# Optimization experiments

Measured on AMD Instinct MI355X. Metric: run time of the kernel, lower is better.

## Reference

```python
import jax, jax.numpy as jnp
import numpy as np

N_NODES = 100000

def _sage_conv(x, edge_index, w_l, b_l, w_r):
    """PyG SAGEConv with mean aggregation:
    out = lin_l(mean_{j in N(i)} x_j) + lin_r(x_i), bias only on lin_l."""
    src, dst = edge_index[0], edge_index[1]
    msgs = x[src]  # [E, d] gather
    agg = jax.ops.segment_sum(msgs, dst, num_segments=N_NODES)  # [N, d]
    cnt = jax.ops.segment_sum(jnp.ones((edge_index.shape[1],), x.dtype), dst,
                              num_segments=N_NODES)
    agg = agg / jnp.maximum(cnt, 1.0)[:, None]  # mean over neighbors
    return agg @ w_l.T + b_l + x @ w_r.T


def setup_inputs() -> dict:
    key = jax.random.key(0)
    ks = jax.random.split(key, 8)
    in_dim, hid_dim, out_dim = 128, 128, 128
    N, E = N_NODES, 1600000
    x = jax.random.normal(ks[0], (N, in_dim), dtype=jnp.float32)
    edge_index = jax.random.randint(ks[1], (2, E), 0, N, dtype=jnp.int64)
    s = 1.0 / np.sqrt(in_dim)
    w1_l = jax.random.uniform(ks[2], (hid_dim, in_dim), jnp.float32, -s, s)
    w1_r = jax.random.uniform(ks[3], (hid_dim, in_dim), jnp.float32, -s, s)
    b1 = jnp.zeros((hid_dim,), jnp.float32)
    s2 = 1.0 / np.sqrt(hid_dim)
    w2_l = jax.random.uniform(ks[4], (out_dim, hid_dim), jnp.float32, -s2, s2)
    w2_r = jax.random.uniform(ks[5], (out_dim, hid_dim), jnp.float32, -s2, s2)
    b2 = jnp.zeros((out_dim,), jnp.float32)
    return {"x": x, "edge_index": edge_index,
            "w1_l": w1_l, "b1": b1, "w1_r": w1_r,
            "w2_l": w2_l, "b2": b2, "w2_r": w2_r}


def reference(x, edge_index, w1_l, b1, w1_r, w2_l, b2, w2_r):
    h = jax.nn.relu(_sage_conv(x, edge_index, w1_l, b1, w1_r))
    # dropout rate 0.0 -> identity (eval-mode reference)
    out = _sage_conv(h, edge_index, w2_l, b2, w2_r)
    return out
```

## Files before the change

### kernel.cpp

```cpp
#include <hip/hip_runtime.h>

#define NDIM 128
#define BKT_SHIFT 9
#define BKT_NODES 512
#define BKT_CAP   12288
#define PART_CHUNK 4096

typedef unsigned short u16;
typedef unsigned char u8;
typedef unsigned int u32;
typedef __attribute__((ext_vector_type(8))) short bf16x8;
typedef __attribute__((ext_vector_type(4))) float f32x4;
typedef __attribute__((ext_vector_type(2))) float f32x2;

__device__ inline u16 f2bf(float f) {
    u32 u = __float_as_uint(f);
    u += 0x7fffu + ((u >> 16) & 1u);
    return (u16)(u >> 16);
}
__device__ inline float bf2f(u16 h) { return __uint_as_float((u32)h << 16); }

__device__ inline u8 f2q(float f) {
    u32 u = __float_as_uint(f);
    u32 s = (u >> 24) & 0x80u;
    float a = __uint_as_float(u & 0x7fffffffu);
    if (a < 0.015625f)
        return (u8)(s | (u32)__float2int_rn(a * 512.f));
    if (a >= 448.f) return (u8)(s | 0x7Eu);
    u32 ur = (u & 0x7fffffffu) + 0x7FFFFu + ((u >> 20) & 1u);
    int e = (int)(ur >> 23) - 127;
    u32 man = (ur >> 20) & 7u;
    u32 r = ((u32)(e + 7) << 3) | man;
    if (r > 0x7Eu) r = 0x7Eu;
    return (u8)(s | r);
}

#if __has_builtin(__builtin_amdgcn_cvt_pk_f32_fp8)
template<bool HI>
__device__ inline f32x2 dq2(u32 w) {
    return __builtin_amdgcn_cvt_pk_f32_fp8((int)w, HI);
}
#else
__device__ inline float dq1(u32 b) {
    int e = (b >> 3) & 15, m = b & 7, s = (b >> 7) & 1;
    int norm = e ? 1 : 0;
    float f = (float)(m + (norm << 3));
    float sc = __uint_as_float((u32)(((e ? e : 1) - 10) + 127) << 23);
    float v = f * sc;
    return s ? -v : v;
}
template<bool HI>
__device__ inline f32x2 dq2(u32 w) {
    u32 sh = HI ? 16 : 0;
    f32x2 r; r.x = dq1((w >> sh) & 0xff); r.y = dq1((w >> (sh + 8)) & 0xff);
    return r;
}
#endif


__global__ __launch_bounds__(256) void partition_kernel(
    const int* __restrict__ ei, int E,
    int* __restrict__ gcur, u32* __restrict__ ebuf) {
    __shared__ int hcnt[256];
    __shared__ int hbase[256];
    const int tid = threadIdx.x;
    const int base = blockIdx.x * PART_CHUNK;
    hcnt[tid] = 0;
    __syncthreads();

    u32 val[16];
    int bkt[16];
    #pragma unroll
    for (int k = 0; k < 16; ++k) {
        int e = base + k * 256 + tid;
        bkt[k] = -1;
        if (e < E) {
            int src = ei[e];
            int dst = ei[(size_t)E + e];
            int b = dst >> BKT_SHIFT;
            bkt[k] = b;
            val[k] = ((u32)src << BKT_SHIFT) | (u32)(dst & (BKT_NODES - 1));
            atomicAdd(&hcnt[b], 1);
        }
    }
    __syncthreads();
    {
        int c = hcnt[tid];
        if (c > 0) hbase[tid] = atomicAdd(&gcur[tid], c);
        hcnt[tid] = 0;
    }
    __syncthreads();
    #pragma unroll
    for (int k = 0; k < 16; ++k) {
        if (bkt[k] >= 0) {
            int b = bkt[k];
            int r = atomicAdd(&hcnt[b], 1);
            int off = hbase[b] + r;
            if (off < BKT_CAP)
                ebuf[(size_t)b * BKT_CAP + off] = val[k];
        }
    }
}

__global__ __launch_bounds__(256) void bucket_csr_kernel(
    const int* __restrict__ gcur, const u32* __restrict__ ebuf,
    int* __restrict__ row_beg, int* __restrict__ degN,
    int* __restrict__ col, int n) {
    __shared__ int deg_l[BKT_NODES];
    __shared__ int pre_l[BKT_NODES];
    __shared__ int cur_l[BKT_NODES];
    __shared__ int wsum[4];
    const int tid = threadIdx.x;
    const int lane = tid & 63, wid = tid >> 6;
    const int b = blockIdx.x;
    const int node0 = b << BKT_SHIFT;
    int cnt = gcur[b];
    if (cnt > BKT_CAP) cnt = BKT_CAP;
    const size_t ebase = (size_t)b * BKT_CAP;

    deg_l[tid] = 0; deg_l[tid + 256] = 0;
    cur_l[tid] = 0; cur_l[tid + 256] = 0;
    __syncthreads();

    for (int i = tid; i < cnt; i += 256)
        atomicAdd(&deg_l[ebuf[ebase + i] & (BKT_NODES - 1)], 1);
    __syncthreads();

    int v0 = deg_l[2 * tid], v1 = deg_l[2 * tid + 1];
    int s = v0 + v1, inc = s;
    #pragma unroll
    for (int d = 1; d < 64; d <<= 1) {
        int t = __shfl_up(inc, d, 64);
        if (lane >= d) inc += t;
    }
    if (lane == 63) wsum[wid] = inc;
    __syncthreads();
    int woff = 0;
    for (int w = 0; w < wid; ++w) woff += wsum[w];
    int ex = woff + (inc - s);
    pre_l[2 * tid] = ex;
    pre_l[2 * tid + 1] = ex + v0;
    __syncthreads();

    #pragma unroll
    for (int p = 0; p < 2; ++p) {
        int idx = tid + p * 256;
        int node = node0 + idx;
        if (node < n) {
            row_beg[node] = (int)ebase + pre_l[idx];
            degN[node]    = deg_l[idx];
        }
    }

    for (int i = tid; i < cnt; i += 256) {
        u32 v = ebuf[ebase + i];
        int d = v & (BKT_NODES - 1);
        int r = atomicAdd(&cur_l[d], 1);
        col[ebase + pre_l[d] + r] = (int)(v >> BKT_SHIFT);
    }
}


__global__ void build_wt_kernel(const float* __restrict__ wl,
                                const float* __restrict__ wr,
                                u16* __restrict__ wth, u16* __restrict__ wtl) {
    int idx = blockIdx.x * blockDim.x + threadIdx.x;
    if (idx >= 128 * 256) return;
    int o = idx >> 8, k = idx & 255;
    float v = (k < 128) ? wl[o * 128 + k] : wr[o * 128 + (k - 128)];
    u16 hi = f2bf(v);
    wth[idx] = hi;
    wtl[idx] = f2bf(v - bf2f(hi));
}


__global__ __launch_bounds__(256) void to_conv_kernel(
    const float* __restrict__ in, u16* __restrict__ outh,
    u8* __restrict__ outq, int n4) {
    int stride = gridDim.x * blockDim.x;
    for (int i = blockIdx.x * blockDim.x + threadIdx.x; i < n4; i += stride) {
        float4 v = *(const float4*)&in[(size_t)i * 4];
        ushort4 o;
        o.x = f2bf(v.x); o.y = f2bf(v.y); o.z = f2bf(v.z); o.w = f2bf(v.w);
        *(ushort4*)&outh[(size_t)i * 4] = o;
        u32 q = (u32)f2q(v.x) | ((u32)f2q(v.y) << 8) |
                ((u32)f2q(v.z) << 16) | ((u32)f2q(v.w) << 24);
        *(u32*)&outq[(size_t)i * 4] = q;
    }
}


__device__ inline void accumq(float acc[8], uint2 u) {
    f32x2 a;
    a = dq2<false>(u.x); acc[0] += a.x; acc[1] += a.y;
    a = dq2<true >(u.x); acc[2] += a.x; acc[3] += a.y;
    a = dq2<false>(u.y); acc[4] += a.x; acc[5] += a.y;
    a = dq2<true >(u.y); acc[6] += a.x; acc[7] += a.y;
}

__global__ __launch_bounds__(256) void aggregate_fp8_kernel(
    const u8* __restrict__ feat, const int* __restrict__ row_beg,
    const int* __restrict__ degN, const int* __restrict__ col,
    u16* __restrict__ aggh, int n) {
    int node = blockIdx.x * 16 + (threadIdx.x >> 4);
    if (node >= n) return;
    int l = threadIdx.x & 15;
    int beg = row_beg[node];
    int dg  = degN[node];
    int end = beg + dg;
    float acc[8] = {0.f, 0.f, 0.f, 0.f, 0.f, 0.f, 0.f, 0.f};
    int j = beg;
    for (; j + 8 <= end; j += 8) {
        int s[8];
        #pragma unroll
        for (int q = 0; q < 8; ++q) s[q] = col[j + q];
        uint2 u[8];
        #pragma unroll
        for (int q = 0; q < 8; ++q)
            u[q] = *(const uint2*)&feat[(size_t)s[q] * NDIM + l * 8];
        #pragma unroll
        for (int q = 0; q < 8; ++q) accumq(acc, u[q]);
    }
    if (j + 4 <= end) {
        int s[4];
        #pragma unroll
        for (int q = 0; q < 4; ++q) s[q] = col[j + q];
        uint2 u[4];
        #pragma unroll
        for (int q = 0; q < 4; ++q)
            u[q] = *(const uint2*)&feat[(size_t)s[q] * NDIM + l * 8];
        #pragma unroll
        for (int q = 0; q < 4; ++q) accumq(acc, u[q]);
        j += 4;
    }
    for (; j < end; ++j) {
        uint2 u = *(const uint2*)&feat[(size_t)col[j] * NDIM + l * 8];
        accumq(acc, u);
    }
    float inv = (dg > 0) ? 1.0f / (float)dg : 0.f;
    u16 hs[8];
    #pragma unroll
    for (int q = 0; q < 8; ++q) hs[q] = f2bf(acc[q] * inv);
    *(ushort4*)&aggh[(size_t)node * NDIM + l * 8]     = make_ushort4(hs[0], hs[1], hs[2], hs[3]);
    *(ushort4*)&aggh[(size_t)node * NDIM + l * 8 + 4] = make_ushort4(hs[4], hs[5], hs[6], hs[7]);
}


__global__ __launch_bounds__(256, 1) void gemm_bstat_kernel(
    const u16* __restrict__ aggh, const u16* __restrict__ selfh,
    const u16* __restrict__ wth, const u16* __restrict__ wtl,
    const float* __restrict__ bias,
    float* __restrict__ outF, u16* __restrict__ outH, u8* __restrict__ outQ,
    int M, int do_relu) {
    const int lane = threadIdx.x & 63;
    const int wid  = threadIdx.x >> 6;
    const int rr = lane & 15, kb = lane >> 4;
    const int ob0 = wid * 32;
    const int ntiles = (M + 15) / 16;
    const int stride = gridDim.x;

    bf16x8 WH0[8], WL0[8], WH1[8], WL1[8];
    {
        const u16* h0 = &wth[(size_t)(ob0 + rr) * 256];
        const u16* l0 = &wtl[(size_t)(ob0 + rr) * 256];
        const u16* h1 = &wth[(size_t)(ob0 + 16 + rr) * 256];
        const u16* l1 = &wtl[(size_t)(ob0 + 16 + rr) * 256];
        #pragma unroll
        for (int ks = 0; ks < 8; ++ks) {
            WH0[ks] = *(const bf16x8*)&h0[ks * 32 + kb * 8];
            WL0[ks] = *(const bf16x8*)&l0[ks * 32 + kb * 8];
            WH1[ks] = *(const bf16x8*)&h1[ks * 32 + kb * 8];
            WL1[ks] = *(const bf16x8*)&l1[ks * 32 + kb * 8];
        }
        #pragma unroll
        for (int ks = 0; ks < 8; ++ks)
            asm volatile("" : "+v"(WH0[ks]), "+v"(WL0[ks]),
                              "+v"(WH1[ks]), "+v"(WL1[ks]));
    }
    const float4 bb0 = *(const float4*)&bias[ob0 + kb * 4];
    const float4 bb1 = *(const float4*)&bias[ob0 + 16 + kb * 4];

    auto loadX = [&](bf16x8* X, int t) {
        int row = t * 16 + rr;
        if (row >= M) row = M - 1;
        const u16* ag = &aggh[(size_t)row * NDIM];
        const u16* sf = &selfh[(size_t)row * NDIM];
        #pragma unroll
        for (int ks = 0; ks < 4; ++ks) X[ks]     = *(const bf16x8*)&ag[ks * 32 + kb * 8];
        #pragma unroll
        for (int ks = 0; ks < 4; ++ks) X[4 + ks] = *(const bf16x8*)&sf[ks * 32 + kb * 8];
    };
    auto pinX = [&](bf16x8* X) {
        #pragma unroll
        for (int i = 0; i < 8; ++i) asm volatile("" : "+v"(X[i]));
    };
    auto computeStore = [&](bf16x8* X, int t) {
        f32x4 acc0 = (f32x4){0.f, 0.f, 0.f, 0.f};
        f32x4 acc1 = (f32x4){0.f, 0.f, 0.f, 0.f};
        #pragma unroll
        for (int ks = 0; ks < 8; ++ks) {
            acc0 = __builtin_amdgcn_mfma_f32_16x16x32_bf16(WH0[ks], X[ks], acc0, 0, 0, 0);
            acc0 = __builtin_amdgcn_mfma_f32_16x16x32_bf16(WL0[ks], X[ks], acc0, 0, 0, 0);
            acc1 = __builtin_amdgcn_mfma_f32_16x16x32_bf16(WH1[ks], X[ks], acc1, 0, 0, 0);
            acc1 = __builtin_amdgcn_mfma_f32_16x16x32_bf16(WL1[ks], X[ks], acc1, 0, 0, 0);
        }
        int node = t * 16 + rr;
        if (node < M) {
            float v0[4], v1[4];
            #pragma unroll
            for (int r = 0; r < 4; ++r) {
                v0[r] = acc0[r] + ((const float*)&bb0)[r];
                v1[r] = acc1[r] + ((const float*)&bb1)[r];
                if (do_relu) { v0[r] = fmaxf(v0[r], 0.f); v1[r] = fmaxf(v1[r], 0.f); }
            }
            const size_t base = (size_t)node * NDIM;
            const int oA = ob0 + kb * 4;
            const int oB = ob0 + 16 + kb * 4;
            if (outF) {
                *(float4*)&outF[base + oA] = make_float4(v0[0], v0[1], v0[2], v0[3]);
                *(float4*)&outF[base + oB] = make_float4(v1[0], v1[1], v1[2], v1[3]);
            }
            if (outH) {
                *(ushort4*)&outH[base + oA] =
                    make_ushort4(f2bf(v0[0]), f2bf(v0[1]), f2bf(v0[2]), f2bf(v0[3]));
                *(ushort4*)&outH[base + oB] =
                    make_ushort4(f2bf(v1[0]), f2bf(v1[1]), f2bf(v1[2]), f2bf(v1[3]));
            }
            if (outQ) {
                *(u32*)&outQ[base + oA] = (u32)f2q(v0[0]) | ((u32)f2q(v0[1]) << 8) |
                                          ((u32)f2q(v0[2]) << 16) | ((u32)f2q(v0[3]) << 24);
                *(u32*)&outQ[base + oB] = (u32)f2q(v1[0]) | ((u32)f2q(v1[1]) << 8) |
                                          ((u32)f2q(v1[2]) << 16) | ((u32)f2q(v1[3]) << 24);
            }
        }
    };

    bf16x8 X0[8], X1[8];
    int t = blockIdx.x;
    if (t >= ntiles) return;
    loadX(X0, t);
    while (true) {
        int tn = t + stride;
        pinX(X0);
        if (tn < ntiles) loadX(X1, tn);
        computeStore(X0, t);
        t = tn;
        if (t >= ntiles) break;
        tn = t + stride;
        pinX(X1);
        if (tn < ntiles) loadX(X0, tn);
        computeStore(X1, t);
        t = tn;
        if (t >= ntiles) break;
    }
}


extern "C" void kernel_launch(void* const* d_in, const int* in_sizes, int n_in,
                              void* d_out, int out_size, void* d_ws, size_t ws_size,
                              hipStream_t stream) {
    const float* x    = (const float*)d_in[0];
    const int*   ei   = (const int*)d_in[1];
    const float* w1_l = (const float*)d_in[2];
    const float* b1   = (const float*)d_in[3];
    const float* w1_r = (const float*)d_in[4];
    const float* w2_l = (const float*)d_in[5];
    const float* b2   = (const float*)d_in[6];
    const float* w2_r = (const float*)d_in[7];
    const int N = in_sizes[0] / NDIM;
    const int E = in_sizes[1] / 2;
    float* out = (float*)d_out;

    const int NB = (N + BKT_NODES - 1) >> BKT_SHIFT;

    char* ws = (char*)d_ws;
    size_t off = 0;
    auto take = [&](size_t bytes) -> char* {
        char* p = ws + off;
        off += (bytes + 255) & ~(size_t)255;
        return p;
    };
    int* row_beg = (int*)take((size_t)N * 4);
    int* degN    = (int*)take((size_t)N * 4);
    int* gcur    = (int*)take((size_t)NB * 4);
    u32* ebuf    = (u32*)take((size_t)NB * BKT_CAP * 4);
    int* colA    = (int*)take((size_t)NB * BKT_CAP * 4);
    u16* wt1h    = (u16*)take(128 * 256 * 2);
    u16* wt1l    = (u16*)take(128 * 256 * 2);
    u16* wt2h    = (u16*)take(128 * 256 * 2);
    u16* wt2l    = (u16*)take(128 * 256 * 2);
    u16* aggh    = (u16*)take((size_t)N * NDIM * 2);
    u16* hh      = (u16*)take((size_t)N * NDIM * 2);
    u16* xh = (u16*)d_out;
    u8*  xq = (u8*)d_out + (size_t)N * NDIM * 2;
    u8*  hq = (u8*)d_out + (size_t)N * NDIM * 3;

    (void)hipMemsetAsync(gcur, 0, (size_t)NB * 4, stream);
    partition_kernel<<<(E + PART_CHUNK - 1) / PART_CHUNK, 256, 0, stream>>>(ei, E, gcur, ebuf);
    bucket_csr_kernel<<<NB, 256, 0, stream>>>(gcur, ebuf, row_beg, degN, colA, N);
    build_wt_kernel<<<128, 256, 0, stream>>>(w1_l, w1_r, wt1h, wt1l);
    build_wt_kernel<<<128, 256, 0, stream>>>(w2_l, w2_r, wt2h, wt2l);
    to_conv_kernel<<<2048, 256, 0, stream>>>(x, xh, xq, N * NDIM / 4);

    const int gblk = 512;
    aggregate_fp8_kernel<<<(N + 15) / 16, 256, 0, stream>>>(xq, row_beg, degN, colA, aggh, N);
    gemm_bstat_kernel<<<gblk, 256, 0, stream>>>(aggh, xh, wt1h, wt1l, b1,
                                                (float*)0, hh, hq, N, 1);
    aggregate_fp8_kernel<<<(N + 15) / 16, 256, 0, stream>>>(hq, row_beg, degN, colA, aggh, N);
    gemm_bstat_kernel<<<gblk, 256, 0, stream>>>(aggh, hh, wt2h, wt2l, b2,
                                                out, (u16*)0, (u8*)0, N, 0);
}
```

Measured before the change: 212.8 us.

## Fuse neighbor aggregation into the GEMM kernel via shared-memory tile

Merges the fp8 mean-aggregation kernel and the dual-weight MFMA GEMM into one persistent kernel. Each block aggregates 16 nodes into a shared-memory bf16 tile, then feeds it straight to the MFMAs, so the intermediate aggregate buffer is never written to or read back from global memory. The cost is that the grid drops to 512 persistent blocks for the latency-bound gather, with a barrier between gather and compute and no cross-tile prefetch. The hq buffer is also moved from the output region into the workspace.

```diff
diff --git a/kernel.cpp b/kernel.cpp
--- a/kernel.cpp
+++ b/kernel.cpp
@@ -198,66 +198,22 @@
     a = dq2<true >(u.y); acc[6] += a.x; acc[7] += a.y;
 }
 
-__global__ __launch_bounds__(256) void aggregate_fp8_kernel(
-    const u8* __restrict__ feat, const int* __restrict__ row_beg,
-    const int* __restrict__ degN, const int* __restrict__ col,
-    u16* __restrict__ aggh, int n) {
-    int node = blockIdx.x * 16 + (threadIdx.x >> 4);
-    if (node >= n) return;
-    int l = threadIdx.x & 15;
-    int beg = row_beg[node];
-    int dg  = degN[node];
-    int end = beg + dg;
-    float acc[8] = {0.f, 0.f, 0.f, 0.f, 0.f, 0.f, 0.f, 0.f};
-    int j = beg;
-    for (; j + 8 <= end; j += 8) {
-        int s[8];
-        #pragma unroll
-        for (int q = 0; q < 8; ++q) s[q] = col[j + q];
-        uint2 u[8];
-        #pragma unroll
-        for (int q = 0; q < 8; ++q)
-            u[q] = *(const uint2*)&feat[(size_t)s[q] * NDIM + l * 8];
-        #pragma unroll
-        for (int q = 0; q < 8; ++q) accumq(acc, u[q]);
-    }
-    if (j + 4 <= end) {
-        int s[4];
-        #pragma unroll
-        for (int q = 0; q < 4; ++q) s[q] = col[j + q];
-        uint2 u[4];
-        #pragma unroll
-        for (int q = 0; q < 4; ++q)
-            u[q] = *(const uint2*)&feat[(size_t)s[q] * NDIM + l * 8];
-        #pragma unroll
-        for (int q = 0; q < 4; ++q) accumq(acc, u[q]);
-        j += 4;
-    }
-    for (; j < end; ++j) {
-        uint2 u = *(const uint2*)&feat[(size_t)col[j] * NDIM + l * 8];
-        accumq(acc, u);
-    }
-    float inv = (dg > 0) ? 1.0f / (float)dg : 0.f;
-    u16 hs[8];
-    #pragma unroll
-    for (int q = 0; q < 8; ++q) hs[q] = f2bf(acc[q] * inv);
-    *(ushort4*)&aggh[(size_t)node * NDIM + l * 8]     = make_ushort4(hs[0], hs[1], hs[2], hs[3]);
-    *(ushort4*)&aggh[(size_t)node * NDIM + l * 8 + 4] = make_ushort4(hs[4], hs[5], hs[6], hs[7]);
-}
-
-
-__global__ __launch_bounds__(256, 1) void gemm_bstat_kernel(
-    const u16* __restrict__ aggh, const u16* __restrict__ selfh,
+__global__ __launch_bounds__(256, 2) void fused_agg_gemm_kernel(
+    const u8* __restrict__ gatherq,
+    const u16* __restrict__ selfh,
+    const int* __restrict__ row_beg, const int* __restrict__ degN,
+    const int* __restrict__ col,
     const u16* __restrict__ wth, const u16* __restrict__ wtl,
     const float* __restrict__ bias,
     float* __restrict__ outF, u16* __restrict__ outH, u8* __restrict__ outQ,
-    int M, int do_relu) {
-    const int lane = threadIdx.x & 63;
-    const int wid  = threadIdx.x >> 6;
+    int n, int do_relu) {
+    __shared__ u16 Ah[16][136];
+    const int tid  = threadIdx.x;
+    const int lane = tid & 63;
+    const int wid  = tid >> 6;
     const int rr = lane & 15, kb = lane >> 4;
     const int ob0 = wid * 32;
-    const int ntiles = (M + 15) / 16;
-    const int stride = gridDim.x;
+    const int ntiles = (n + 15) / 16;
 
     bf16x8 WH0[8], WL0[8], WH1[8], WL1[8];
     {
@@ -280,78 +236,119 @@
     const float4 bb0 = *(const float4*)&bias[ob0 + kb * 4];
     const float4 bb1 = *(const float4*)&bias[ob0 + 16 + kb * 4];
 
-    auto loadX = [&](bf16x8* X, int t) {
-        int row = t * 16 + rr;
-        if (row >= M) row = M - 1;
-        const u16* ag = &aggh[(size_t)row * NDIM];
-        const u16* sf = &selfh[(size_t)row * NDIM];
-        #pragma unroll
-        for (int ks = 0; ks < 4; ++ks) X[ks]     = *(const bf16x8*)&ag[ks * 32 + kb * 8];
-        #pragma unroll
-        for (int ks = 0; ks < 4; ++ks) X[4 + ks] = *(const bf16x8*)&sf[ks * 32 + kb * 8];
-    };
-    auto pinX = [&](bf16x8* X) {
-        #pragma unroll
-        for (int i = 0; i < 8; ++i) asm volatile("" : "+v"(X[i]));
-    };
-    auto computeStore = [&](bf16x8* X, int t) {
-        f32x4 acc0 = (f32x4){0.f, 0.f, 0.f, 0.f};
-        f32x4 acc1 = (f32x4){0.f, 0.f, 0.f, 0.f};
-        #pragma unroll
-        for (int ks = 0; ks < 8; ++ks) {
-            acc0 = __builtin_amdgcn_mfma_f32_16x16x32_bf16(WH0[ks], X[ks], acc0, 0, 0, 0);
-            acc0 = __builtin_amdgcn_mfma_f32_16x16x32_bf16(WL0[ks], X[ks], acc0, 0, 0, 0);
-            acc1 = __builtin_amdgcn_mfma_f32_16x16x32_bf16(WH1[ks], X[ks], acc1, 0, 0, 0);
-            acc1 = __builtin_amdgcn_mfma_f32_16x16x32_bf16(WL1[ks], X[ks], acc1, 0, 0, 0);
-        }
-        int node = t * 16 + rr;
-        if (node < M) {
-            float v0[4], v1[4];
+    for (int t = blockIdx.x; t < ntiles; t += gridDim.x) {
+        bf16x8 XS[4];
+        {
+            int row = t * 16 + rr;
+            if (row >= n) row = n - 1;
+            const u16* sf = &selfh[(size_t)row * NDIM];
             #pragma unroll
-            for (int r = 0; r < 4; ++r) {
-                v0[r] = acc0[r] + ((const float*)&bb0)[r];
-                v1[r] = acc1[r] + ((const float*)&bb1)[r];
-                if (do_relu) { v0[r] = fmaxf(v0[r], 0.f); v1[r] = fmaxf(v1[r], 0.f); }
+            for (int ks = 0; ks < 4; ++ks)
+                XS[ks] = *(const bf16x8*)&sf[ks * 32 + kb * 8];
+        }
+
+        {
+            const int nl = tid >> 4, l = tid & 15;
+            const int node = t * 16 + nl;
+            float acc[8] = {0.f, 0.f, 0.f, 0.f, 0.f, 0.f, 0.f, 0.f};
+            if (node < n) {
+                int beg = row_beg[node];
+                int dg  = degN[node];
+                int end = beg + dg;
+                int j = beg;
+                for (; j + 8 <= end; j += 8) {
+                    int s[8];
+                    #pragma unroll
+                    for (int q = 0; q < 8; ++q) s[q] = col[j + q];
+                    uint2 u[8];
+                    #pragma unroll
+                    for (int q = 0; q < 8; ++q)
+                        u[q] = *(const uint2*)&gatherq[(size_t)s[q] * NDIM + l * 8];
+                    #pragma unroll
+                    for (int q = 0; q < 8; ++q) accumq(acc, u[q]);
+                }
+                if (j + 4 <= end) {
+                    int s[4];
+                    #pragma unroll
+                    for (int q = 0; q < 4; ++q) s[q] = col[j + q];
+                    uint2 u[4];
+                    #pragma unroll
+                    for (int q = 0; q < 4; ++q)
+                        u[q] = *(const uint2*)&gatherq[(size_t)s[q] * NDIM + l * 8];
+                    #pragma unroll
+                    for (int q = 0; q < 4; ++q) accumq(acc, u[q]);
+                    j += 4;
+                }
+                for (; j < end; ++j) {
+                    uint2 u = *(const uint2*)&gatherq[(size_t)col[j] * NDIM + l * 8];
+                    accumq(acc, u);
+                }
+                float inv = (dg > 0) ? 1.0f / (float)dg : 0.f;
+                #pragma unroll
+                for (int q = 0; q < 8; ++q) acc[q] *= inv;
             }
-            const size_t base = (size_t)node * NDIM;
-            const int oA = ob0 + kb * 4;
-            const int oB = ob0 + 16 + kb * 4;
-            if (outF) {
-                *(float4*)&outF[base + oA] = make_float4(v0[0], v0[1], v0[2], v0[3]);
-                *(float4*)&outF[base + oB] = make_float4(v1[0], v1[1], v1[2], v1[3]);
+            u32 w0 = (u32)f2bf(acc[0]) | ((u32)f2bf(acc[1]) << 16);
+            u32 w1 = (u32)f2bf(acc[2]) | ((u32)f2bf(acc[3]) << 16);
+            u32 w2 = (u32)f2bf(acc[4]) | ((u32)f2bf(acc[5]) << 16);
+            u32 w3 = (u32)f2bf(acc[6]) | ((u32)f2bf(acc[7]) << 16);
+            *(uint4*)&Ah[nl][l * 8] = make_uint4(w0, w1, w2, w3);
+        }
+        __syncthreads();
+
+        {
+            bf16x8 XA[4];
+            #pragma unroll
+            for (int ks = 0; ks < 4; ++ks)
+                XA[ks] = *(const bf16x8*)&Ah[rr][ks * 32 + kb * 8];
+
+            f32x4 acc0 = (f32x4){0.f, 0.f, 0.f, 0.f};
+            f32x4 acc1 = (f32x4){0.f, 0.f, 0.f, 0.f};
+            #pragma unroll
+            for (int ks = 0; ks < 4; ++ks) {
+                acc0 = __builtin_amdgcn_mfma_f32_16x16x32_bf16(WH0[ks], XA[ks], acc0, 0, 0, 0);
+                acc0 = __builtin_amdgcn_mfma_f32_16x16x32_bf16(WL0[ks], XA[ks], acc0, 0, 0, 0);
+                acc1 = __builtin_amdgcn_mfma_f32_16x16x32_bf16(WH1[ks], XA[ks], acc1, 0, 0, 0);
+                acc1 = __builtin_amdgcn_mfma_f32_16x16x32_bf16(WL1[ks], XA[ks], acc1, 0, 0, 0);
             }
-            if (outH) {
-                *(ushort4*)&outH[base + oA] =
-                    make_ushort4(f2bf(v0[0]), f2bf(v0[1]), f2bf(v0[2]), f2bf(v0[3]));
-                *(ushort4*)&outH[base + oB] =
-                    make_ushort4(f2bf(v1[0]), f2bf(v1[1]), f2bf(v1[2]), f2bf(v1[3]));
+            #pragma unroll
+            for (int ks = 0; ks < 4; ++ks) {
+                acc0 = __builtin_amdgcn_mfma_f32_16x16x32_bf16(WH0[4 + ks], XS[ks], acc0, 0, 0, 0);
+                acc0 = __builtin_amdgcn_mfma_f32_16x16x32_bf16(WL0[4 + ks], XS[ks], acc0, 0, 0, 0);
+                acc1 = __builtin_amdgcn_mfma_f32_16x16x32_bf16(WH1[4 + ks], XS[ks], acc1, 0, 0, 0);
+                acc1 = __builtin_amdgcn_mfma_f32_16x16x32_bf16(WL1[4 + ks], XS[ks], acc1, 0, 0, 0);
             }
-            if (outQ) {
-                *(u32*)&outQ[base + oA] = (u32)f2q(v0[0]) | ((u32)f2q(v0[1]) << 8) |
-                                          ((u32)f2q(v0[2]) << 16) | ((u32)f2q(v0[3]) << 24);
-                *(u32*)&outQ[base + oB] = (u32)f2q(v1[0]) | ((u32)f2q(v1[1]) << 8) |
-                                          ((u32)f2q(v1[2]) << 16) | ((u32)f2q(v1[3]) << 24);
+
+            int node = t * 16 + rr;
+            if (node < n) {
+                float v0[4], v1[4];
+                #pragma unroll
+                for (int r = 0; r < 4; ++r) {
+                    v0[r] = acc0[r] + ((const float*)&bb0)[r];
+                    v1[r] = acc1[r] + ((const float*)&bb1)[r];
+                    if (do_relu) { v0[r] = fmaxf(v0[r], 0.f); v1[r] = fmaxf(v1[r], 0.f); }
+                }
+                const size_t base = (size_t)node * NDIM;
+                const int oA = ob0 + kb * 4;
+                const int oB = ob0 + 16 + kb * 4;
+                if (outF) {
+                    *(float4*)&outF[base + oA] = make_float4(v0[0], v0[1], v0[2], v0[3]);
+                    *(float4*)&outF[base + oB] = make_float4(v1[0], v1[1], v1[2], v1[3]);
+                }
+                if (outH) {
+                    *(ushort4*)&outH[base + oA] =
+                        make_ushort4(f2bf(v0[0]), f2bf(v0[1]), f2bf(v0[2]), f2bf(v0[3]));
+                    *(ushort4*)&outH[base + oB] =
+                        make_ushort4(f2bf(v1[0]), f2bf(v1[1]), f2bf(v1[2]), f2bf(v1[3]));
+                }
+                if (outQ) {
+                    *(u32*)&outQ[base + oA] = (u32)f2q(v0[0]) | ((u32)f2q(v0[1]) << 8) |
+                                              ((u32)f2q(v0[2]) << 16) | ((u32)f2q(v0[3]) << 24);
+                    *(u32*)&outQ[base + oB] = (u32)f2q(v1[0]) | ((u32)f2q(v1[1]) << 8) |
+                                              ((u32)f2q(v1[2]) << 16) | ((u32)f2q(v1[3]) << 24);
+                }
             }
         }
-    };
-
-    bf16x8 X0[8], X1[8];
-    int t = blockIdx.x;
-    if (t >= ntiles) return;
-    loadX(X0, t);
-    while (true) {
-        int tn = t + stride;
-        pinX(X0);
-        if (tn < ntiles) loadX(X1, tn);
-        computeStore(X0, t);
-        t = tn;
-        if (t >= ntiles) break;
-        tn = t + stride;
-        pinX(X1);
-        if (tn < ntiles) loadX(X0, tn);
-        computeStore(X1, t);
-        t = tn;
-        if (t >= ntiles) break;
+        __syncthreads();
     }
 }
 
@@ -389,11 +386,10 @@
     u16* wt1l    = (u16*)take(128 * 256 * 2);
     u16* wt2h    = (u16*)take(128 * 256 * 2);
     u16* wt2l    = (u16*)take(128 * 256 * 2);
-    u16* aggh    = (u16*)take((size_t)N * NDIM * 2);
     u16* hh      = (u16*)take((size_t)N * NDIM * 2);
+    u8*  hq      = (u8*)take((size_t)N * NDIM);
     u16* xh = (u16*)d_out;
     u8*  xq = (u8*)d_out + (size_t)N * NDIM * 2;
-    u8*  hq = (u8*)d_out + (size_t)N * NDIM * 3;
 
     (void)hipMemsetAsync(gcur, 0, (size_t)NB * 4, stream);
     partition_kernel<<<(E + PART_CHUNK - 1) / PART_CHUNK, 256, 0, stream>>>(ei, E, gcur, ebuf);
@@ -403,10 +399,10 @@
     to_conv_kernel<<<2048, 256, 0, stream>>>(x, xh, xq, N * NDIM / 4);
 
     const int gblk = 512;
-    aggregate_fp8_kernel<<<(N + 15) / 16, 256, 0, stream>>>(xq, row_beg, degN, colA, aggh, N);
-    gemm_bstat_kernel<<<gblk, 256, 0, stream>>>(aggh, xh, wt1h, wt1l, b1,
-                                                (float*)0, hh, hq, N, 1);
-    aggregate_fp8_kernel<<<(N + 15) / 16, 256, 0, stream>>>(hq, row_beg, degN, colA, aggh, N);
-    gemm_bstat_kernel<<<gblk, 256, 0, stream>>>(aggh, hh, wt2h, wt2l, b2,
-                                                out, (u16*)0, (u8*)0, N, 0);
-}
+    fused_agg_gemm_kernel<<<gblk, 256, 0, stream>>>(xq, xh, row_beg, degN, colA,
+                                                    wt1h, wt1l, b1,
+                                                    (float*)0, hh, hq, N, 1);
+    fused_agg_gemm_kernel<<<gblk, 256, 0, stream>>>(hq, hh, row_beg, degN, colA,
+                                                    wt2h, wt2l, b2,
+                                                    out, (u16*)0, (u8*)0, N, 0);
+}
```

Result: slower. 256.1 us (+20.3%).

## Stage GEMM activation tiles through LDS with async global-to-LDS loads

Applied to the files above, without the earlier changes.

The weight-stationary GEMM kernel now loads each 16-row activation tile (aggregated and self features) once per block. It uses global_load_lds directly into a double-buffered, XOR-swizzled shared-memory buffer, and each wave reads the tile back from LDS. Before, every wave loaded the full tile from global memory on its own, so each tile was fetched four times. Launch bounds now allow two blocks per CU. The cost is a block-wide barrier per tile and LDS traffic, and the tail of a tile is loaded past M without clamping.

```diff
diff --git a/kernel.cpp b/kernel.cpp
--- a/kernel.cpp
+++ b/kernel.cpp
@@ -56,6 +56,12 @@
     return r;
 }
 #endif
+
+__device__ __forceinline__ void gl_lds16(const void* g, void* l) {
+    __builtin_amdgcn_global_load_lds(
+        (const __attribute__((address_space(1))) void*)g,
+        (__attribute__((address_space(3))) void*)l, 16, 0, 0);
+}
 
 
 __global__ __launch_bounds__(256) void partition_kernel(
@@ -246,14 +252,16 @@
 }
 
 
-__global__ __launch_bounds__(256, 1) void gemm_bstat_kernel(
+__global__ __launch_bounds__(256, 2) void gemm_wstat_lds_kernel(
     const u16* __restrict__ aggh, const u16* __restrict__ selfh,
     const u16* __restrict__ wth, const u16* __restrict__ wtl,
     const float* __restrict__ bias,
     float* __restrict__ outF, u16* __restrict__ outH, u8* __restrict__ outQ,
     int M, int do_relu) {
-    const int lane = threadIdx.x & 63;
-    const int wid  = threadIdx.x >> 6;
+    __shared__ u16 Abuf[2][4096];
+    const int tid  = threadIdx.x;
+    const int lane = tid & 63;
+    const int wid  = tid >> 6;
     const int rr = lane & 15, kb = lane >> 4;
     const int ob0 = wid * 32;
     const int ntiles = (M + 15) / 16;
@@ -280,29 +288,54 @@
     const float4 bb0 = *(const float4*)&bias[ob0 + kb * 4];
     const float4 bb1 = *(const float4*)&bias[ob0 + 16 + kb * 4];
 
-    auto loadX = [&](bf16x8* X, int t) {
-        int row = t * 16 + rr;
-        if (row >= M) row = M - 1;
-        const u16* ag = &aggh[(size_t)row * NDIM];
-        const u16* sf = &selfh[(size_t)row * NDIM];
-        #pragma unroll
-        for (int ks = 0; ks < 4; ++ks) X[ks]     = *(const bf16x8*)&ag[ks * 32 + kb * 8];
-        #pragma unroll
-        for (int ks = 0; ks < 4; ++ks) X[4 + ks] = *(const bf16x8*)&sf[ks * 32 + kb * 8];
+    int srcoff[2];
+    int reg_[2];
+    int ldsoff[2];
+    #pragma unroll
+    for (int is = 0; is < 2; ++is) {
+        int c = wid * 128 + is * 64 + lane;
+        int cc = c & 255;
+        int sc = cc ^ ((cc >> 4) & 7);
+        srcoff[is] = sc * 16;
+        reg_[is]   = c >> 8;
+        ldsoff[is] = (wid * 128 + is * 64) * 8;
+    }
+
+    auto stage = [&](int buf, int t) {
+        const char* ga = (const char*)aggh  + (size_t)t * 4096;
+        const char* gs = (const char*)selfh + (size_t)t * 4096;
+        #pragma unroll
+        for (int is = 0; is < 2; ++is) {
+            const char* g = (reg_[is] ? gs : ga) + srcoff[is];
+            gl_lds16(g, &Abuf[buf][ldsoff[is]]);
+        }
     };
-    auto pinX = [&](bf16x8* X) {
-        #pragma unroll
-        for (int i = 0; i < 8; ++i) asm volatile("" : "+v"(X[i]));
-    };
-    auto computeStore = [&](bf16x8* X, int t) {
+
+    auto computeStore = [&](int buf, int t) {
+        const char* sb = (const char*)&Abuf[buf][0];
+        const int sw = (rr & 7) << 4;
+        bf16x8 XA[4], XS[4];
+        #pragma unroll
+        for (int ks = 0; ks < 4; ++ks) {
+            int a = rr * 256 + ks * 64 + kb * 16;
+            XA[ks] = *(const bf16x8*)(sb + (a ^ sw));
+            XS[ks] = *(const bf16x8*)(sb + 4096 + (a ^ sw));
+        }
         f32x4 acc0 = (f32x4){0.f, 0.f, 0.f, 0.f};
         f32x4 acc1 = (f32x4){0.f, 0.f, 0.f, 0.f};
         #pragma unroll
-        for (int ks = 0; ks < 8; ++ks) {
-            acc0 = __builtin_amdgcn_mfma_f32_16x16x32_bf16(WH0[ks], X[ks], acc0, 0, 0, 0);
-            acc0 = __builtin_amdgcn_mfma_f32_16x16x32_bf16(WL0[ks], X[ks], acc0, 0, 0, 0);
-            acc1 = __builtin_amdgcn_mfma_f32_16x16x32_bf16(WH1[ks], X[ks], acc1, 0, 0, 0);
-            acc1 = __builtin_amdgcn_mfma_f32_16x16x32_bf16(WL1[ks], X[ks], acc1, 0, 0, 0);
+        for (int ks = 0; ks < 4; ++ks) {
+            acc0 = __builtin_amdgcn_mfma_f32_16x16x32_bf16(WH0[ks], XA[ks], acc0, 0, 0, 0);
+            acc0 = __builtin_amdgcn_mfma_f32_16x16x32_bf16(WL0[ks], XA[ks], acc0, 0, 0, 0);
+            acc1 = __builtin_amdgcn_mfma_f32_16x16x32_bf16(WH1[ks], XA[ks], acc1, 0, 0, 0);
+            acc1 = __builtin_amdgcn_mfma_f32_16x16x32_bf16(WL1[ks], XA[ks], acc1, 0, 0, 0);
+        }
+        #pragma unroll
+        for (int ks = 0; ks < 4; ++ks) {
+            acc0 = __builtin_amdgcn_mfma_f32_16x16x32_bf16(WH0[4 + ks], XS[ks], acc0, 0, 0, 0);
+            acc0 = __builtin_amdgcn_mfma_f32_16x16x32_bf16(WL0[4 + ks], XS[ks], acc0, 0, 0, 0);
+            acc1 = __builtin_amdgcn_mfma_f32_16x16x32_bf16(WH1[4 + ks], XS[ks], acc1, 0, 0, 0);
+            acc1 = __builtin_amdgcn_mfma_f32_16x16x32_bf16(WL1[4 + ks], XS[ks], acc1, 0, 0, 0);
         }
         int node = t * 16 + rr;
         if (node < M) {
@@ -335,21 +368,17 @@
         }
     };
 
-    bf16x8 X0[8], X1[8];
     int t = blockIdx.x;
     if (t >= ntiles) return;
-    loadX(X0, t);
+    int cur = 0;
+    stage(0, t);
+    __syncthreads();
     while (true) {
         int tn = t + stride;
-        pinX(X0);
-        if (tn < ntiles) loadX(X1, tn);
-        computeStore(X0, t);
-        t = tn;
-        if (t >= ntiles) break;
-        tn = t + stride;
-        pinX(X1);
-        if (tn < ntiles) loadX(X0, tn);
-        computeStore(X1, t);
+        if (tn < ntiles) stage(cur ^ 1, tn);
+        computeStore(cur, t);
+        __syncthreads();
+        cur ^= 1;
         t = tn;
         if (t >= ntiles) break;
     }
@@ -404,9 +433,9 @@
 
     const int gblk = 512;
     aggregate_fp8_kernel<<<(N + 15) / 16, 256, 0, stream>>>(xq, row_beg, degN, colA, aggh, N);
-    gemm_bstat_kernel<<<gblk, 256, 0, stream>>>(aggh, xh, wt1h, wt1l, b1,
-                                                (float*)0, hh, hq, N, 1);
+    gemm_wstat_lds_kernel<<<gblk, 256, 0, stream>>>(aggh, xh, wt1h, wt1l, b1,
+                                                    (float*)0, hh, hq, N, 1);
     aggregate_fp8_kernel<<<(N + 15) / 16, 256, 0, stream>>>(hq, row_beg, degN, colA, aggh, N);
-    gemm_bstat_kernel<<<gblk, 256, 0, stream>>>(aggh, hh, wt2h, wt2l, b2,
-                                                out, (u16*)0, (u8*)0, N, 0);
-}
+    gemm_wstat_lds_kernel<<<gblk, 256, 0, stream>>>(aggh, hh, wt2h, wt2l, b2,
+                                                    out, (u16*)0, (u8*)0, N, 0);
+}
```

Result: faster. 187.2 us, median of 2 (-12.1%).
